# Performance work log

Hardware: AMD Instinct MI355X
Metric: run time of the kernel (lower is better)

## Reference

```python
import jax, jax.numpy as jnp
import numpy as np

ALPHA = 0.5

def pairwise_sqdist(a, b):
    # a: [B,N,3], b: [B,M,3] -> [B,N,M] squared euclidean distances
    a2 = jnp.sum(a * a, axis=-1)[:, :, None]
    b2 = jnp.sum(b * b, axis=-1)[:, None, :]
    ab = jnp.einsum('bnd,bmd->bnm', a, b)
    return jnp.maximum(a2 + b2 - 2.0 * ab, 0.0)

def setup_inputs() -> dict:
    key = jax.random.key(0)
    k1, k2, k3, k4, k5 = jax.random.split(key, 5)
    B, N_UP, N_SEED, N_GT, N_RAD = 4, 8192, 2048, 8192, 1024
    return {
        'pc_up':   jax.random.normal(k1, (B, N_UP, 3), dtype=jnp.float32),
        'pc_seed': jax.random.normal(k2, (B, N_SEED, 3), dtype=jnp.float32),
        'pc_conf': jax.random.uniform(k3, (B, N_RAD, 1), dtype=jnp.float32),
        'pc2':     jax.random.normal(k4, (B, N_GT, 3), dtype=jnp.float32),
        'pc3':     jax.random.normal(k5, (B, N_RAD, 3), dtype=jnp.float32),
    }

def reference(pc_up, pc_seed, pc_conf, pc2, pc3):
    # --- confidence score target: exp(-min euclidean dist from radar to GT) ---
    d_rad_gt = pairwise_sqdist(pc3, pc2)                      # [B,N_rad,N_gt]
    min_dist = jnp.sqrt(jnp.min(d_rad_gt, axis=-1))           # [B,N_rad]
    gt_scores = jnp.exp(-min_dist)[..., None]                 # [B,N_rad,1]
    conf_loss = jnp.mean((pc_conf - gt_scores) ** 2)

    # --- Chamfer (squared distances, as standard ChamferDistance kernels) ---
    d_up_gt = pairwise_sqdist(pc_up, pc2)                     # [B,N_up,N_gt]
    dist1 = jnp.min(d_up_gt, axis=2)                          # up -> gt
    dist2 = jnp.min(d_up_gt, axis=1)                          # gt -> up
    chamfer_up = 0.5 * jnp.mean(dist1) + 2.0 * jnp.mean(dist2)

    # --- EMD surrogate: nearest-neighbor matching cost, sqrt(dist).mean() ---
    # (original uses an approximate auction-based emdFunction; nearest-neighbor
    # assignment is the standard differentiable reference surrogate)
    emd_loss = jnp.mean(jnp.sqrt(dist1))

    final_loss = ALPHA * chamfer_up + ALPHA * conf_loss + emd_loss
    return final_loss
```

## Files before the change

kernel.cpp:

```cpp
#include <hip/hip_runtime.h>
#include <math.h>


#define THREADS 256

typedef __attribute__((ext_vector_type(8))) short s8v;
typedef __attribute__((ext_vector_type(16))) float f16v;

__device__ __forceinline__ unsigned short f2bf(float x) {
    unsigned u = __float_as_uint(x);
    u += 0x7FFFu + ((u >> 16) & 1u);
    return (unsigned short)(u >> 16);
}
__device__ __forceinline__ float bf2f(unsigned short h) {
    return __uint_as_float((unsigned)h << 16);
}

__global__ __launch_bounds__(THREADS) void init_ws_kernel(unsigned int* ws) {
    int i = blockIdx.x * THREADS + threadIdx.x;
    if (i < 69632) ws[i] = 0x7F800000u;
}

__global__ __launch_bounds__(THREADS, 2) void
mfma_pass_kernel(const float* __restrict__ pc_up, const float* __restrict__ pc2,
                 const float* __restrict__ pc3,
                 float* ws1, float* ws2, float* ws3) {
    __shared__ unsigned short tiles[16][2][32][8];

    int bid = blockIdx.x;
    const float* Ap;
    const float* Bp;
    float* outmin;
    int NA;
    if (bid < 1024) {
        Ap = pc_up; Bp = pc2; outmin = ws1; NA = 8192;
    } else if (bid < 2048) {
        bid -= 1024; Ap = pc2; Bp = pc_up; outmin = ws2; NA = 8192;
    } else {
        bid -= 2048; Ap = pc3; Bp = pc2; outmin = ws3; NA = 1024;
    }
    const int rb = bid >> 4, sp = bid & 15;
    const int NB = 8192;
    const int rowBase = rb * 512;
    const int batch = rowBase / NA;
    const int colBase = sp * 512;

    const float* bsrc = Bp + ((size_t)batch * NB + colBase) * 3;
    for (int c = threadIdx.x; c < 512; c += THREADS) {
        float x = bsrc[c * 3 + 0], y = bsrc[c * 3 + 1], z = bsrc[c * 3 + 2];
        float ux = -2.f * x, uy = -2.f * y, uz = -2.f * z;
        unsigned short uxh = f2bf(ux), uyh = f2bf(uy), uzh = f2bf(uz);
        unsigned short uxl = f2bf(ux - bf2f(uxh));
        unsigned short uyl = f2bf(uy - bf2f(uyh));
        unsigned short uzl = f2bf(uz - bf2f(uzh));
        float b2 = x * x + y * y + z * z;
        unsigned short b2h = f2bf(b2);
        unsigned short b2l = f2bf(b2 - bf2f(b2h));
        int ct = c >> 5, cc = c & 31;
        s8v h0 = {(short)uxh, (short)uyh, (short)uzh, (short)uxh,
                  (short)uyh, (short)uzh, (short)uxl, (short)uyl};
        s8v h1 = {(short)uzl, (short)b2h, (short)b2l, 0, 0, 0, 0, 0};
        *(s8v*)&tiles[ct][0][cc][0] = h0;
        *(s8v*)&tiles[ct][1][cc][0] = h1;
    }

    const int lane = threadIdx.x & 63;
    const int w = threadIdx.x >> 6;
    const int half = lane >> 5;
    const int rl = lane & 31;
    s8v afrag[4];
    float a2[4];
#pragma unroll
    for (int f = 0; f < 4; ++f) {
        int row = rowBase + (w * 4 + f) * 32 + rl;
        float x = Ap[row * 3 + 0], y = Ap[row * 3 + 1], z = Ap[row * 3 + 2];
        unsigned short xh = f2bf(x), yh = f2bf(y), zh = f2bf(z);
        unsigned short xl = f2bf(x - bf2f(xh));
        unsigned short yl = f2bf(y - bf2f(yh));
        unsigned short zl = f2bf(z - bf2f(zh));
        a2[f] = x * x + y * y + z * z;
        s8v fr0 = {(short)xh, (short)yh, (short)zh, (short)xl,
                   (short)yl, (short)zl, (short)xh, (short)yh};
        s8v fr1 = {(short)zh, (short)0x3F80, (short)0x3F80, 0, 0, 0, 0, 0};
        afrag[f] = half ? fr1 : fr0;
    }
    __syncthreads();

    f16v zero;
#pragma unroll
    for (int i = 0; i < 16; ++i) zero[i] = 0.0f;
    float m[4] = {INFINITY, INFINITY, INFINITY, INFINITY};

#pragma unroll 2
    for (int t = 0; t < 16; ++t) {
        s8v bfrag = *(const s8v*)&tiles[t][half][rl][0];
#pragma unroll
        for (int f = 0; f < 4; ++f) {
            f16v d = __builtin_amdgcn_mfma_f32_32x32x16_bf16(
                bfrag, afrag[f], zero, 0, 0, 0);
            float u0 = fminf(fminf(d[0], d[1]), d[2]);
            float u1 = fminf(fminf(d[3], d[4]), d[5]);
            float u2 = fminf(fminf(d[6], d[7]), d[8]);
            float u3 = fminf(fminf(d[9], d[10]), d[11]);
            float u4 = fminf(fminf(d[12], d[13]), d[14]);
            float v0 = fminf(fminf(u0, u1), u2);
            float v1 = fminf(fminf(u3, u4), d[15]);
            m[f] = fminf(fminf(m[f], v0), v1);
        }
    }

#pragma unroll
    for (int f = 0; f < 4; ++f) {
        float v = fminf(m[f], __shfl_xor(m[f], 32, 64));
        float d = fmaxf(a2[f] + v, 0.0f);
        if (half == 0) {
            atomicMin((unsigned int*)&outmin[rowBase + (w * 4 + f) * 32 + rl],
                      __float_as_uint(d));
        }
    }
}

__global__ __launch_bounds__(THREADS) void
reduce_kernel(const float* __restrict__ ws1, const float* __restrict__ ws2,
              const float* __restrict__ ws3, const float* __restrict__ conf,
              float* __restrict__ out) {
    const int gid = blockIdx.x * THREADS + threadIdx.x;

    const float w1 = 0.25f / 32768.0f;
    const float wq = 1.0f / 32768.0f;
    const float w2 = 1.0f / 32768.0f;
    const float w3 = 0.5f / 4096.0f;

    float v1 = ws1[gid];
    float v2 = ws2[gid];
    float s = w1 * v1 + wq * sqrtf(v1) + w2 * v2;
    if (gid < 4096) {
        float diff = conf[gid] - expf(-sqrtf(ws3[gid]));
        s += w3 * diff * diff;
    }

    __shared__ float wsum[4];
    const int lane = threadIdx.x & 63;
    const int wave = threadIdx.x >> 6;
    for (int off = 32; off > 0; off >>= 1) s += __shfl_down(s, off, 64);
    if (lane == 0) wsum[wave] = s;
    __syncthreads();
    if (threadIdx.x == 0)
        atomicAdd(out, wsum[0] + wsum[1] + wsum[2] + wsum[3]);
}

extern "C" void kernel_launch(void* const* d_in, const int* in_sizes, int n_in,
                              void* d_out, int out_size, void* d_ws, size_t ws_size,
                              hipStream_t stream) {
    const float* pc_up   = (const float*)d_in[0];
    const float* pc_conf = (const float*)d_in[2];
    const float* pc2     = (const float*)d_in[3];
    const float* pc3     = (const float*)d_in[4];

    float* ws1 = (float*)d_ws;
    float* ws2 = ws1 + 32768;
    float* ws3 = ws2 + 32768;

    init_ws_kernel<<<273, THREADS, 0, stream>>>((unsigned int*)d_ws);
    mfma_pass_kernel<<<2176, THREADS, 0, stream>>>(pc_up, pc2, pc3, ws1, ws2, ws3);
    reduce_kernel<<<128, THREADS, 0, stream>>>(ws1, ws2, ws3, pc_conf,
                                               (float*)d_out);
}
```

Baseline: 83.06 us.

## Replace atomicMin workspace init with per-split partial minima reduced in final kernel

The init kernel and global atomicMin are removed. Each block now writes its row minima to a private partial buffer indexed by column split, and the reduce kernel takes the min across the splits. The column split also changes from 16 to 8, so each block processes 1024 columns and the grid is halved. This saves one kernel launch and the atomic traffic, but the reduce kernel now reads 8x more data and the grid has fewer blocks to spread across the GPU.

New measurement: 83.38 us. Within noise of the previous version (+0.4%).

```diff
diff --git a/kernel.cpp b/kernel.cpp
--- a/kernel.cpp
+++ b/kernel.cpp
@@ -3,6 +3,7 @@
 
 
 #define THREADS 256
+#define NSPLIT 8
 
 typedef __attribute__((ext_vector_type(8))) short s8v;
 typedef __attribute__((ext_vector_type(16))) float f16v;
@@ -16,37 +17,32 @@
     return __uint_as_float((unsigned)h << 16);
 }
 
-__global__ __launch_bounds__(THREADS) void init_ws_kernel(unsigned int* ws) {
-    int i = blockIdx.x * THREADS + threadIdx.x;
-    if (i < 69632) ws[i] = 0x7F800000u;
-}
-
 __global__ __launch_bounds__(THREADS, 2) void
 mfma_pass_kernel(const float* __restrict__ pc_up, const float* __restrict__ pc2,
                  const float* __restrict__ pc3,
-                 float* ws1, float* ws2, float* ws3) {
-    __shared__ unsigned short tiles[16][2][32][8];
+                 float* p1, float* p2, float* p3) {
+    __shared__ unsigned short tiles[32][2][32][8];
 
     int bid = blockIdx.x;
     const float* Ap;
     const float* Bp;
-    float* outmin;
-    int NA;
-    if (bid < 1024) {
-        Ap = pc_up; Bp = pc2; outmin = ws1; NA = 8192;
-    } else if (bid < 2048) {
-        bid -= 1024; Ap = pc2; Bp = pc_up; outmin = ws2; NA = 8192;
+    float* part;
+    int NA, rowsTot;
+    if (bid < 512) {
+        Ap = pc_up; Bp = pc2; part = p1; NA = 8192; rowsTot = 32768;
+    } else if (bid < 1024) {
+        bid -= 512; Ap = pc2; Bp = pc_up; part = p2; NA = 8192; rowsTot = 32768;
     } else {
-        bid -= 2048; Ap = pc3; Bp = pc2; outmin = ws3; NA = 1024;
+        bid -= 1024; Ap = pc3; Bp = pc2; part = p3; NA = 1024; rowsTot = 4096;
     }
-    const int rb = bid >> 4, sp = bid & 15;
+    const int rb = bid >> 3, sp = bid & 7;
     const int NB = 8192;
     const int rowBase = rb * 512;
     const int batch = rowBase / NA;
-    const int colBase = sp * 512;
+    const int colBase = sp * 1024;
 
     const float* bsrc = Bp + ((size_t)batch * NB + colBase) * 3;
-    for (int c = threadIdx.x; c < 512; c += THREADS) {
+    for (int c = threadIdx.x; c < 1024; c += THREADS) {
         float x = bsrc[c * 3 + 0], y = bsrc[c * 3 + 1], z = bsrc[c * 3 + 2];
         float ux = -2.f * x, uy = -2.f * y, uz = -2.f * z;
         unsigned short uxh = f2bf(ux), uyh = f2bf(uy), uzh = f2bf(uz);
@@ -92,7 +88,7 @@
     float m[4] = {INFINITY, INFINITY, INFINITY, INFINITY};
 
 #pragma unroll 2
-    for (int t = 0; t < 16; ++t) {
+    for (int t = 0; t < 32; ++t) {
         s8v bfrag = *(const s8v*)&tiles[t][half][rl][0];
 #pragma unroll
         for (int f = 0; f < 4; ++f) {
@@ -113,16 +109,14 @@
     for (int f = 0; f < 4; ++f) {
         float v = fminf(m[f], __shfl_xor(m[f], 32, 64));
         float d = fmaxf(a2[f] + v, 0.0f);
-        if (half == 0) {
-            atomicMin((unsigned int*)&outmin[rowBase + (w * 4 + f) * 32 + rl],
-                      __float_as_uint(d));
-        }
+        if (half == 0)
+            part[sp * rowsTot + rowBase + (w * 4 + f) * 32 + rl] = d;
     }
 }
 
 __global__ __launch_bounds__(THREADS) void
-reduce_kernel(const float* __restrict__ ws1, const float* __restrict__ ws2,
-              const float* __restrict__ ws3, const float* __restrict__ conf,
+reduce_kernel(const float* __restrict__ p1, const float* __restrict__ p2,
+              const float* __restrict__ p3, const float* __restrict__ conf,
               float* __restrict__ out) {
     const int gid = blockIdx.x * THREADS + threadIdx.x;
 
@@ -131,11 +125,19 @@
     const float w2 = 1.0f / 32768.0f;
     const float w3 = 0.5f / 4096.0f;
 
-    float v1 = ws1[gid];
-    float v2 = ws2[gid];
+    float v1 = INFINITY, v2 = INFINITY;
+#pragma unroll
+    for (int sp = 0; sp < NSPLIT; ++sp) {
+        v1 = fminf(v1, p1[sp * 32768 + gid]);
+        v2 = fminf(v2, p2[sp * 32768 + gid]);
+    }
     float s = w1 * v1 + wq * sqrtf(v1) + w2 * v2;
     if (gid < 4096) {
-        float diff = conf[gid] - expf(-sqrtf(ws3[gid]));
+        float v3 = INFINITY;
+#pragma unroll
+        for (int sp = 0; sp < NSPLIT; ++sp)
+            v3 = fminf(v3, p3[sp * 4096 + gid]);
+        float diff = conf[gid] - expf(-sqrtf(v3));
         s += w3 * diff * diff;
     }
 
@@ -157,12 +159,11 @@
     const float* pc2     = (const float*)d_in[3];
     const float* pc3     = (const float*)d_in[4];
 
-    float* ws1 = (float*)d_ws;
-    float* ws2 = ws1 + 32768;
-    float* ws3 = ws2 + 32768;
+    float* p1 = (float*)d_ws;
+    float* p2 = p1 + NSPLIT * 32768;
+    float* p3 = p2 + NSPLIT * 32768;
 
-    init_ws_kernel<<<273, THREADS, 0, stream>>>((unsigned int*)d_ws);
-    mfma_pass_kernel<<<2176, THREADS, 0, stream>>>(pc_up, pc2, pc3, ws1, ws2, ws3);
-    reduce_kernel<<<128, THREADS, 0, stream>>>(ws1, ws2, ws3, pc_conf,
+    mfma_pass_kernel<<<1088, THREADS, 0, stream>>>(pc_up, pc2, pc3, p1, p2, p3);
+    reduce_kernel<<<128, THREADS, 0, stream>>>(p1, p2, p3, pc_conf,
                                                (float*)d_out);
 }
```
